# Performance work log

Measured on AMD Instinct MI355X. Metric: run time of the kernel, lower is better.

Reference implementation:

```python
import jax, jax.numpy as jnp
import numpy as np

THRESHOLD = 1.0
DECAY = 0.95
REFRACTORY = 2.0
LATERAL_SCALE = 0.1


def setup_inputs() -> dict:
    key = jax.random.key(0)
    k1, k2, k3, k4 = jax.random.split(key, 4)
    B, T, I, H, O = 64, 128, 512, 2048, 512
    x = jax.random.normal(k1, (B, T, I), dtype=jnp.float32)
    input_weights = jax.random.normal(k2, (I, H), dtype=jnp.float32) * 0.1
    hidden_weights = jax.random.normal(k3, (H, O), dtype=jnp.float32) * 0.1
    lateral_inhibition = jax.random.normal(k4, (H, H), dtype=jnp.float32) * 0.01
    return {"x": x, "input_weights": input_weights,
            "hidden_weights": hidden_weights,
            "lateral_inhibition": lateral_inhibition}


def reference(x, input_weights, hidden_weights, lateral_inhibition):
    B, T, I = x.shape
    H = input_weights.shape[1]

    def step(carry, xt):
        mp, rc = carry  # membrane potentials, refractory counters: [B, H]
        input_current = xt @ input_weights            # [B, H]
        active = (rc <= 0).astype(mp.dtype)
        mp = DECAY * mp + input_current * active
        spikes = (mp >= THRESHOLD).astype(mp.dtype)   # [B, H]
        mp = mp * (1.0 - spikes)
        rc = jnp.maximum(rc - 1.0, 0.0) + spikes * REFRACTORY
        mp = mp - LATERAL_SCALE * (spikes @ lateral_inhibition)
        out = spikes @ hidden_weights                 # [B, O]
        return (mp, rc), out

    mp0 = jnp.zeros((B, H), dtype=x.dtype)
    rc0 = jnp.zeros((B, H), dtype=x.dtype)
    xs = jnp.swapaxes(x, 0, 1)  # [T, B, I]
    _, outs = jax.lax.scan(step, (mp0, rc0), xs)
    return jnp.swapaxes(outs, 0, 1)  # [B, T, O]
```

## Files before the change

### kernel.cpp

```cpp
#include <hip/hip_runtime.h>

static constexpr int NB = 64;
static constexpr int NT = 128;
static constexpr int NI = 512;
static constexpr int NH = 2048;
static constexpr int NO = 512;

typedef __attribute__((ext_vector_type(8))) short short8;
typedef __attribute__((ext_vector_type(4))) float f32x4;
typedef __attribute__((ext_vector_type(2))) unsigned long long ull2;
typedef __attribute__((ext_vector_type(4))) unsigned int u32x4;

__device__ __forceinline__ unsigned short bf16_rne(float f) {
  unsigned int u = __float_as_uint(f);
  u += 0x7FFFu + ((u >> 16) & 1u);
  return (unsigned short)(u >> 16);
}
__device__ __forceinline__ float bf16_to_f32(unsigned short h) {
  return __uint_as_float(((unsigned int)h) << 16);
}

__global__ __launch_bounds__(512) void k_clear_mask(unsigned int* __restrict__ m) {
  int idx = blockIdx.x * 512 + threadIdx.x;
  __hip_atomic_store(&m[idx], 0u, __ATOMIC_RELAXED, __HIP_MEMORY_SCOPE_AGENT);
}

__global__ __launch_bounds__(256) void k_split_L(const float* __restrict__ L,
                                                 unsigned short* __restrict__ LThi,
                                                 unsigned short* __restrict__ LTlo) {
  __shared__ float tile[32][33];
  const int h0 = blockIdx.x * 32;
  const int c0 = blockIdx.y * 32;
  const int lx = threadIdx.x & 31, ly = threadIdx.x >> 5;
#pragma unroll
  for (int i = 0; i < 4; ++i) {
    int r = ly + i * 8;
    tile[r][lx] = L[(size_t)(h0 + r) * NH + c0 + lx];
  }
  __syncthreads();
#pragma unroll
  for (int i = 0; i < 4; ++i) {
    int r = ly + i * 8;
    float v = tile[lx][r];
    unsigned short hi = bf16_rne(v);
    float lo = v - bf16_to_f32(hi);
    LThi[(size_t)(c0 + r) * NH + h0 + lx] = hi;
    LTlo[(size_t)(c0 + r) * NH + h0 + lx] = bf16_rne(lo);
  }
}

__global__ __launch_bounds__(256) void k_t_Wh(const float* __restrict__ Wh,
                                              unsigned short* __restrict__ WhT) {
  __shared__ float tile[32][33];
  const int h0 = blockIdx.x * 32;
  const int o0 = blockIdx.y * 32;
  const int lx = threadIdx.x & 31, ly = threadIdx.x >> 5;
#pragma unroll
  for (int i = 0; i < 4; ++i) {
    int r = ly + i * 8;
    tile[r][lx] = Wh[(size_t)(h0 + r) * NO + o0 + lx];
  }
  __syncthreads();
#pragma unroll
  for (int i = 0; i < 4; ++i) {
    int r = ly + i * 8;
    WhT[(size_t)(o0 + r) * NH + h0 + lx] = bf16_rne(tile[lx][r]);
  }
}

__global__ __launch_bounds__(256) void k_ic_gemm(const float* __restrict__ X,
                                                 const float* __restrict__ W,
                                                 float* __restrict__ IC) {
  __shared__ float As[16][132];
  __shared__ float Bs[16][132];
  const int m0 = blockIdx.x * 128, n0 = blockIdx.y * 128;
  const int tid = threadIdx.x;
  const int tx = tid & 15, ty = tid >> 4;
  float acc[8][8] = {};
  for (int kt = 0; kt < NI; kt += 16) {
#pragma unroll
    for (int j = 0; j < 2; ++j) {
      int f = tid * 2 + j;
      int r = f >> 2, k4 = (f & 3) * 4;
      float4 va = *(const float4*)&X[(size_t)(m0 + r) * NI + kt + k4];
      As[k4 + 0][r] = va.x; As[k4 + 1][r] = va.y;
      As[k4 + 2][r] = va.z; As[k4 + 3][r] = va.w;
      int kk = f >> 5, c4 = (f & 31) * 4;
      *(float4*)&Bs[kk][c4] = *(const float4*)&W[(size_t)(kt + kk) * NH + n0 + c4];
    }
    __syncthreads();
    for (int kk = 0; kk < 16; ++kk) {
      float4 a0 = *(const float4*)&As[kk][ty * 8];
      float4 a1 = *(const float4*)&As[kk][ty * 8 + 4];
      float4 b0 = *(const float4*)&Bs[kk][tx * 4];
      float4 b1 = *(const float4*)&Bs[kk][64 + tx * 4];
      float a_[8] = {a0.x, a0.y, a0.z, a0.w, a1.x, a1.y, a1.z, a1.w};
      float b_[8] = {b0.x, b0.y, b0.z, b0.w, b1.x, b1.y, b1.z, b1.w};
#pragma unroll
      for (int i = 0; i < 8; ++i)
#pragma unroll
        for (int j = 0; j < 8; ++j) acc[i][j] = fmaf(a_[i], b_[j], acc[i][j]);
    }
    __syncthreads();
  }
#pragma unroll
  for (int i = 0; i < 8; ++i) {
    int m = m0 + ty * 8 + i;
    int tt = m & (NT - 1), bb = m >> 7;
    float* op = &IC[((size_t)tt * NB + bb) * NH + n0];
    float4 v0 = {acc[i][0], acc[i][1], acc[i][2], acc[i][3]};
    float4 v1 = {acc[i][4], acc[i][5], acc[i][6], acc[i][7]};
    *(float4*)&op[tx * 4] = v0;
    *(float4*)&op[64 + tx * 4] = v1;
  }
}

__global__ __launch_bounds__(256, 1) void k_scan(const float* __restrict__ IC,
                                                 const unsigned short* __restrict__ LThi,
                                                 const unsigned short* __restrict__ LTlo,
                                                 unsigned int* __restrict__ mask) {
  __shared__ unsigned long long lut[16];
  __shared__ unsigned char sstage[4 * 64 * 48];
  __shared__ f32x4 spart[2 * 4 * 2 * 64];
  const int tid = threadIdx.x;
  const int cs = blockIdx.x >> 1;
  const int mh = blockIdx.x & 1;
  const int wave = tid >> 6, lane = tid & 63;
  const int n = lane & 15, q = lane >> 4;
  const int wsel = q >> 1, par = q & 1;
  if (tid < 16) {
    unsigned long long v = 0;
    if (tid & 1) v |= 0x3F80ull;
    if (tid & 2) v |= 0x3F80ull << 16;
    if (tid & 4) v |= 0x3F80ull << 32;
    if (tid & 8) v |= 0x3F80ull << 48;
    lut[tid] = v;
  }
  const int b_u = tid >> 3, cp = tid & 7;
  float mp0 = 0.f, mp1 = 0.f, rc0 = 0.f, rc1 = 0.f;

  short8 Bh[16], Bl[16];
  {
    const int c = cs * 16 + n;
#pragma unroll
    for (int ks = 0; ks < 16; ++ks) {
      int k0 = wave * 512 + ks * 32 + q * 8;
      Bh[ks] = *(const short8*)(LThi + (size_t)c * NH + k0);
      Bl[ks] = *(const short8*)(LTlo + (size_t)c * NH + k0);
    }
  }
  __syncthreads();

  for (int t = 0; t < NT; ++t) {
    const float* icp = &IC[((size_t)t * NB + mh * 32 + b_u) * NH + cs * 16 + cp * 2];
    float ic0 = icp[0], ic1 = icp[1];
    float lat0 = 0.f, lat1 = 0.f;
    const int pp = t & 1;
    if (t > 0) {
      const unsigned int* pbase = mask + (size_t)(t - 1) * 8192 +
                                  (wave * 32 + (lane >> 1)) * 64 + mh * 32 +
                                  (lane & 1) * 16;
      u32x4 w0, w1, w2, w3;
      for (;;) {
        asm volatile(
            "global_load_dwordx4 %0, %4, off sc0 sc1\n\t"
            "global_load_dwordx4 %1, %4, off offset:16 sc0 sc1\n\t"
            "global_load_dwordx4 %2, %4, off offset:32 sc0 sc1\n\t"
            "global_load_dwordx4 %3, %4, off offset:48 sc0 sc1\n\t"
            "s_waitcnt vmcnt(0)"
            : "=&v"(w0), "=&v"(w1), "=&v"(w2), "=&v"(w3)
            : "v"(pbase)
            : "memory");
        unsigned int conj = (w0.x & w0.y) & (w0.z & w0.w);
        conj &= (w1.x & w1.y) & (w1.z & w1.w);
        conj &= (w2.x & w2.y) & (w2.z & w2.w);
        conj &= (w3.x & w3.y) & (w3.z & w3.w);
        if (conj & 0x10000u) break;
        __builtin_amdgcn_s_sleep(1);
      }
      unsigned int v[16] = {w0.x, w0.y, w0.z, w0.w, w1.x, w1.y, w1.z, w1.w,
                            w2.x, w2.y, w2.z, w2.w, w3.x, w3.y, w3.z, w3.w};
      unsigned long long p[4];
#pragma unroll
      for (int i = 0; i < 4; ++i)
        p[i] = (unsigned long long)(v[i * 4 + 0] & 0xFFFFu) |
               ((unsigned long long)(v[i * 4 + 1] & 0xFFFFu) << 16) |
               ((unsigned long long)(v[i * 4 + 2] & 0xFFFFu) << 32) |
               ((unsigned long long)(v[i * 4 + 3] & 0xFFFFu) << 48);
      unsigned char* sbase = sstage + (wave * 64 + lane) * 48;
      *(ull2*)sbase = ull2{p[0], p[1]};
      *(ull2*)(sbase + 16) = ull2{p[2], p[3]};
      __asm__ volatile("s_waitcnt lgkmcnt(0)" ::: "memory");
      f32x4 acc[2] = {{0, 0, 0, 0}, {0, 0, 0, 0}};
      const unsigned char* smb = sstage + wave * (64 * 48);
#pragma unroll
      for (int ks = 0; ks < 16; ++ks) {
#pragma unroll
        for (int mt = 0; mt < 2; ++mt) {
          unsigned char by = smb[(ks * 4 + wsel * 2 + mt) * 48 + n * 2 + par];
          union { unsigned long long d[2]; short8 s; } a;
          a.d[0] = lut[by & 15];
          a.d[1] = lut[by >> 4];
          acc[mt] = __builtin_amdgcn_mfma_f32_16x16x32_bf16(a.s, Bl[ks], acc[mt], 0, 0, 0);
          acc[mt] = __builtin_amdgcn_mfma_f32_16x16x32_bf16(a.s, Bh[ks], acc[mt], 0, 0, 0);
        }
      }
#pragma unroll
      for (int mt = 0; mt < 2; ++mt)
        spart[((pp * 4 + wave) * 2 + mt) * 64 + lane] = acc[mt];
      __syncthreads();
      {
        const float* sp = (const float*)spart;
        int mt = b_u >> 4, mit = b_u & 15;
        int lidx = (mit >> 2) * 16, reg = mit & 3;
        int ca = cp * 2;
#pragma unroll
        for (int w = 0; w < 4; ++w) {
          int base = ((pp * 4 + w) * 2 + mt) * 64 + lidx;
          lat0 += sp[(size_t)(base + ca) * 4 + reg];
          lat1 += sp[(size_t)(base + ca + 1) * 4 + reg];
        }
      }
    }
    unsigned int word;
    {
      mp0 -= 0.1f * lat0;
      mp1 -= 0.1f * lat1;
      float a0 = (rc0 <= 0.f) ? 1.f : 0.f;
      float a1 = (rc1 <= 0.f) ? 1.f : 0.f;
      mp0 = 0.95f * mp0 + ic0 * a0;
      mp1 = 0.95f * mp1 + ic1 * a1;
      float s0 = (mp0 >= 1.f) ? 1.f : 0.f;
      float s1 = (mp1 >= 1.f) ? 1.f : 0.f;
      mp0 = (s0 != 0.f) ? 0.f : mp0;
      mp1 = (s1 != 0.f) ? 0.f : mp1;
      rc0 = fmaxf(rc0 - 1.f, 0.f) + 2.f * s0;
      rc1 = fmaxf(rc1 - 1.f, 0.f) + 2.f * s1;
      unsigned int bits = ((s0 != 0.f) ? 1u : 0u) | ((s1 != 0.f) ? 2u : 0u);
      word = bits << (cp * 2);
    }
    word |= (unsigned int)__builtin_amdgcn_ds_swizzle((int)word, 0x041F);
    word |= (unsigned int)__builtin_amdgcn_ds_swizzle((int)word, 0x081F);
    word |= (unsigned int)__builtin_amdgcn_ds_swizzle((int)word, 0x101F);
    if ((lane & 7) == 0) {
      int b = mh * 32 + wave * 8 + (lane >> 3);
      __hip_atomic_store(&mask[(size_t)t * 8192 + cs * 64 + b], word | 0x10000u,
                         __ATOMIC_RELAXED, __HIP_MEMORY_SCOPE_AGENT);
    }
  }
}

__global__ __launch_bounds__(256) void k_out_gemm(const unsigned int* __restrict__ mask,
                                                  const unsigned short* __restrict__ WhT,
                                                  float* __restrict__ out) {
  __shared__ unsigned long long lut[16];
  __shared__ unsigned short smask16[8192];
  const int tid = threadIdx.x;
  if (tid < 16) {
    unsigned long long v = 0;
    if (tid & 1) v |= 0x3F80ull;
    if (tid & 2) v |= 0x3F80ull << 16;
    if (tid & 4) v |= 0x3F80ull << 32;
    if (tid & 8) v |= 0x3F80ull << 48;
    lut[tid] = v;
  }
  const int t0 = blockIdx.x;
  {
    const unsigned int* pb = mask + (size_t)t0 * 8192 + tid * 32;
    u32x4 a0, a1, a2, a3, a4, a5, a6, a7;
    asm volatile(
        "global_load_dwordx4 %0, %8, off sc0 sc1\n\t"
        "global_load_dwordx4 %1, %8, off offset:16 sc0 sc1\n\t"
        "global_load_dwordx4 %2, %8, off offset:32 sc0 sc1\n\t"
        "global_load_dwordx4 %3, %8, off offset:48 sc0 sc1\n\t"
        "global_load_dwordx4 %4, %8, off offset:64 sc0 sc1\n\t"
        "global_load_dwordx4 %5, %8, off offset:80 sc0 sc1\n\t"
        "global_load_dwordx4 %6, %8, off offset:96 sc0 sc1\n\t"
        "global_load_dwordx4 %7, %8, off offset:112 sc0 sc1\n\t"
        "s_waitcnt vmcnt(0)"
        : "=&v"(a0), "=&v"(a1), "=&v"(a2), "=&v"(a3),
          "=&v"(a4), "=&v"(a5), "=&v"(a6), "=&v"(a7)
        : "v"(pb)
        : "memory");
    u32x4 aa[8] = {a0, a1, a2, a3, a4, a5, a6, a7};
    unsigned int* sm = (unsigned int*)&smask16[tid * 32];
#pragma unroll
    for (int i = 0; i < 8; ++i) {
      sm[i * 2 + 0] = (aa[i].x & 0xFFFFu) | ((aa[i].y & 0xFFFFu) << 16);
      sm[i * 2 + 1] = (aa[i].z & 0xFFFFu) | ((aa[i].w & 0xFFFFu) << 16);
    }
  }
  __syncthreads();
  const int wave = tid >> 6, lane = tid & 63;
  const int n0 = blockIdx.y * 64 + wave * 16;
  const int n = lane & 15;
  const unsigned char* smb = (const unsigned char*)smask16;
  f32x4 acc[4] = {{0,0,0,0},{0,0,0,0},{0,0,0,0},{0,0,0,0}};
  for (int ks = 0; ks < 64; ++ks) {
    int k0 = ks * 32 + ((lane >> 4) << 3);
    union { unsigned long long d[2]; short8 s; } bfr;
    bfr.d[0] = *(const unsigned long long*)(WhT + (size_t)(n0 + n) * NH + k0);
    bfr.d[1] = *(const unsigned long long*)(WhT + (size_t)(n0 + n) * NH + k0 + 4);
    int wc = k0 >> 4, pr = (k0 >> 3) & 1;
#pragma unroll
    for (int mt = 0; mt < 4; ++mt) {
      int b = mt * 16 + n;
      unsigned char by = smb[(wc * 64 + b) * 2 + pr];
      union { unsigned long long d[2]; short8 s; } a;
      a.d[0] = lut[by & 15];
      a.d[1] = lut[by >> 4];
      acc[mt] = __builtin_amdgcn_mfma_f32_16x16x32_bf16(a.s, bfr.s, acc[mt], 0, 0, 0);
    }
  }
#pragma unroll
  for (int mt = 0; mt < 4; ++mt)
#pragma unroll
    for (int r = 0; r < 4; ++r) {
      int b = mt * 16 + ((lane >> 4) << 2) + r;
      out[((size_t)b * NT + t0) * NO + n0 + n] = acc[mt][r];
    }
}

extern "C" void kernel_launch(void* const* d_in, const int* in_sizes, int n_in,
                              void* d_out, int out_size, void* d_ws, size_t ws_size,
                              hipStream_t stream) {
  const float* x   = (const float*)d_in[0];
  const float* Win = (const float*)d_in[1];
  const float* Wh  = (const float*)d_in[2];
  const float* L   = (const float*)d_in[3];
  float* out = (float*)d_out;

  char* ws = (char*)d_ws;
  size_t off = 0;
  auto alloc = [&](size_t bytes) -> void* {
    void* p = ws + off;
    off = (off + bytes + 255) & ~(size_t)255;
    return p;
  };
  unsigned short* LThi = (unsigned short*)alloc((size_t)NH * NH * 2);
  unsigned short* LTlo = (unsigned short*)alloc((size_t)NH * NH * 2);
  unsigned short* WhT  = (unsigned short*)alloc((size_t)NO * NH * 2);
  float* IC            = (float*)alloc((size_t)NT * NB * NH * 4);
  unsigned int* mask   = (unsigned int*)alloc((size_t)NT * 8192 * 4);

  hipLaunchKernelGGL(k_clear_mask, dim3(NT * 8192 / 512), dim3(512), 0, stream, mask);
  hipLaunchKernelGGL(k_split_L, dim3(64, 64), dim3(256), 0, stream, L, LThi, LTlo);
  hipLaunchKernelGGL(k_t_Wh, dim3(64, 16), dim3(256), 0, stream, Wh, WhT);
  hipLaunchKernelGGL(k_ic_gemm, dim3(64, 16), dim3(256), 0, stream, x, Win, IC);
  {
    const float* icp = IC;
    const unsigned short* lh = LThi;
    const unsigned short* ll = LTlo;
    unsigned int* mk = mask;
    void* kargs[] = {(void*)&icp, (void*)&lh, (void*)&ll, (void*)&mk};
    hipLaunchCooperativeKernel((void*)k_scan, dim3(256), dim3(256), kargs, 0, stream);
  }
  hipLaunchKernelGGL(k_out_gemm, dim3(128, 8), dim3(256), 0, stream,
                     (const unsigned int*)mask, (const unsigned short*)WhT, out);
}
```

Measured before the change: 727.7 us.

## Split recurrent scan across 512 blocks with two blocks per CU

Adds a k_scan2 variant of the cooperative time-step scan in which each block handles 16 batch rows instead of 32, doubling the grid to 512 blocks with launch bounds allowing two blocks per CU. It uses a 256-entry byte LUT to expand spike bits into bf16 MFMA operands, one element per thread, and polls half as much mask data per step. The host checks occupancy and falls back to the original kernel if two blocks cannot be co-resident. This aims to raise per-step parallelism and latency hiding in the serial scan, at the cost of register pressure from holding the B fragments under a tighter register budget, and more blocks participating in the cross-block flag synchronisation.

```diff
diff --git a/kernel.cpp b/kernel.cpp
--- a/kernel.cpp
+++ b/kernel.cpp
@@ -112,6 +112,115 @@
     float4 v1 = {acc[i][4], acc[i][5], acc[i][6], acc[i][7]};
     *(float4*)&op[tx * 4] = v0;
     *(float4*)&op[64 + tx * 4] = v1;
+  }
+}
+
+__global__ __launch_bounds__(256, 2) void k_scan2(const float* __restrict__ IC,
+                                                  const unsigned short* __restrict__ LThi,
+                                                  const unsigned short* __restrict__ LTlo,
+                                                  unsigned int* __restrict__ mask) {
+  __shared__ ull2 lut[256];
+  __shared__ unsigned int sstage[4 * 256];
+  __shared__ f32x4 spart[2 * 4 * 64];
+  const int tid = threadIdx.x;
+  const int cs = blockIdx.x >> 2;
+  const int bq = blockIdx.x & 3;
+  const int wave = tid >> 6, lane = tid & 63;
+  const int n = lane & 15, q = lane >> 4;
+  {
+    int i = tid;
+    unsigned long long d0 = 0, d1 = 0;
+#pragma unroll
+    for (int j = 0; j < 4; ++j) {
+      if ((i >> j) & 1) d0 |= 0x3F80ull << (16 * j);
+      if ((i >> (j + 4)) & 1) d1 |= 0x3F80ull << (16 * j);
+    }
+    lut[i] = ull2{d0, d1};
+  }
+  const int b_l = tid >> 4, c_l = tid & 15;
+  float mp = 0.f, rc = 0.f;
+
+  short8 Bh[16], Bl[16];
+  {
+    const int c = cs * 16 + n;
+#pragma unroll
+    for (int ks = 0; ks < 16; ++ks) {
+      int k0 = wave * 512 + ks * 32 + q * 8;
+      Bh[ks] = *(const short8*)(LThi + (size_t)c * NH + k0);
+      Bl[ks] = *(const short8*)(LTlo + (size_t)c * NH + k0);
+    }
+  }
+  __syncthreads();
+
+  for (int t = 0; t < NT; ++t) {
+    const float ic = IC[((size_t)t * NB + bq * 16 + b_l) * NH + cs * 16 + c_l];
+    float lat = 0.f;
+    const int pp = t & 1;
+    if (t > 0) {
+      const unsigned int* pbase = mask + (size_t)(t - 1) * 8192 +
+                                  (wave * 32 + (lane >> 1)) * 64 + bq * 16 +
+                                  (lane & 1) * 8;
+      u32x4 w0, w1;
+      for (;;) {
+        asm volatile(
+            "global_load_dwordx4 %0, %2, off sc0 sc1\n\t"
+            "global_load_dwordx4 %1, %2, off offset:16 sc0 sc1\n\t"
+            "s_waitcnt vmcnt(0)"
+            : "=&v"(w0), "=&v"(w1)
+            : "v"(pbase)
+            : "memory");
+        unsigned int conj = (w0.x & w0.y) & (w0.z & w0.w) &
+                            (w1.x & w1.y) & (w1.z & w1.w);
+        if (conj & 0x10000u) break;
+        __builtin_amdgcn_s_sleep(1);
+      }
+      u32x4 dw;
+      dw.x = (w0.x & 0xFFFFu) | (w0.y << 16);
+      dw.y = (w0.z & 0xFFFFu) | (w0.w << 16);
+      dw.z = (w1.x & 0xFFFFu) | (w1.y << 16);
+      dw.w = (w1.z & 0xFFFFu) | (w1.w << 16);
+      *(u32x4*)((unsigned char*)&sstage[wave * 256] + lane * 16) = dw;
+      __asm__ volatile("s_waitcnt lgkmcnt(0)" ::: "memory");
+      f32x4 acch = {0, 0, 0, 0}, accl = {0, 0, 0, 0};
+      const unsigned char* smb = (const unsigned char*)&sstage[wave * 256];
+#pragma unroll
+      for (int ks = 0; ks < 16; ++ks) {
+        unsigned char by = smb[ks * 64 + (q >> 1) * 32 + n * 2 + (q & 1)];
+        union { ull2 d; short8 s; } a;
+        a.d = lut[by];
+        acch = __builtin_amdgcn_mfma_f32_16x16x32_bf16(a.s, Bh[ks], acch, 0, 0, 0);
+        accl = __builtin_amdgcn_mfma_f32_16x16x32_bf16(a.s, Bl[ks], accl, 0, 0, 0);
+      }
+      f32x4 acc = acch + accl;
+      spart[(pp * 4 + wave) * 64 + lane] = acc;
+      __syncthreads();
+      {
+        const float* sp = (const float*)spart;
+        int lidx = (b_l >> 2) * 16 + c_l, reg = b_l & 3;
+#pragma unroll
+        for (int w = 0; w < 4; ++w)
+          lat += sp[(size_t)((pp * 4 + w) * 64 + lidx) * 4 + reg];
+      }
+    }
+    unsigned int word;
+    {
+      mp -= 0.1f * lat;
+      float a0 = (rc <= 0.f) ? 1.f : 0.f;
+      mp = 0.95f * mp + ic * a0;
+      float s = (mp >= 1.f) ? 1.f : 0.f;
+      mp = (s != 0.f) ? 0.f : mp;
+      rc = fmaxf(rc - 1.f, 0.f) + 2.f * s;
+      word = (s != 0.f) ? (1u << c_l) : 0u;
+    }
+    word |= (unsigned int)__builtin_amdgcn_ds_swizzle((int)word, 0x041F);
+    word |= (unsigned int)__builtin_amdgcn_ds_swizzle((int)word, 0x081F);
+    word |= (unsigned int)__builtin_amdgcn_ds_swizzle((int)word, 0x101F);
+    word |= (unsigned int)__builtin_amdgcn_ds_swizzle((int)word, 0x201F);
+    if (n == 0) {
+      __hip_atomic_store(&mask[(size_t)t * 8192 + cs * 64 + bq * 16 + b_l],
+                         word | 0x10000u, __ATOMIC_RELAXED,
+                         __HIP_MEMORY_SCOPE_AGENT);
+    }
   }
 }
 
@@ -138,7 +247,6 @@
   }
   const int b_u = tid >> 3, cp = tid & 7;
   float mp0 = 0.f, mp1 = 0.f, rc0 = 0.f, rc1 = 0.f;
-
   short8 Bh[16], Bl[16];
   {
     const int c = cs * 16 + n;
@@ -150,7 +258,6 @@
     }
   }
   __syncthreads();
-
   for (int t = 0; t < NT; ++t) {
     const float* icp = &IC[((size_t)t * NB + mh * 32 + b_u) * NH + cs * 16 + cp * 2];
     float ic0 = icp[0], ic1 = icp[1];
@@ -353,7 +460,16 @@
     const unsigned short* ll = LTlo;
     unsigned int* mk = mask;
     void* kargs[] = {(void*)&icp, (void*)&lh, (void*)&ll, (void*)&mk};
-    hipLaunchCooperativeKernel((void*)k_scan, dim3(256), dim3(256), kargs, 0, stream);
+    int maxb = 0;
+    hipError_t e = hipOccupancyMaxActiveBlocksPerMultiprocessor(
+        &maxb, (const void*)k_scan2, 256, 0);
+    if (e == hipSuccess && maxb >= 2) {
+      hipLaunchCooperativeKernel((void*)k_scan2, dim3(512), dim3(256), kargs, 0,
+                                 stream);
+    } else {
+      hipLaunchCooperativeKernel((void*)k_scan, dim3(256), dim3(256), kargs, 0,
+                                 stream);
+    }
   }
   hipLaunchKernelGGL(k_out_gemm, dim3(128, 8), dim3(256), 0, stream,
                      (const unsigned int*)mask, (const unsigned short*)WhT, out);
```

Measured after the change: 727.5 us. No clear change (-0.0%).
